# Kernel optimization log

Hardware: AMD Instinct MI355X
Metric: run time of the kernel (lower is better)

Reference implementation:

```python
import jax, jax.numpy as jnp
import numpy as np

D_MODEL = 1024
NUM_HEADS = 16
HDIM = D_MODEL // NUM_HEADS
THETA = 10000.0


def setup_inputs() -> dict:
    key = jax.random.key(0)
    ks = jax.random.split(key, 5)
    bs, seq = 4, 2048
    std = np.sqrt(2.0 / (D_MODEL + D_MODEL))
    def w(k):
        # trunc_normal approximated by clipped normal (same distribution family)
        return jnp.clip(std * jax.random.normal(k, (D_MODEL, D_MODEL), jnp.float32), -3 * std, 3 * std)
    return {
        "x": jax.random.normal(ks[0], (bs, seq, D_MODEL), jnp.float32),
        "Wq": w(ks[1]), "Wk": w(ks[2]), "Wv": w(ks[3]), "Wo": w(ks[4]),
        "token_positions": jnp.arange(seq, dtype=jnp.int64),
    }


def _rope(x, token_positions):
    # x: (bs, H, S, hdim); rotate even/odd interleaved pairs
    inv_freq = THETA ** (-2.0 * jnp.arange(HDIM // 2, dtype=jnp.float32) / HDIM)
    freqs = token_positions.astype(jnp.float32)[:, None] * inv_freq[None, :]  # (S, hdim/2)
    cos, sin = jnp.cos(freqs), jnp.sin(freqs)
    x_even, x_odd = x[..., 0::2], x[..., 1::2]
    out_even = x_even * cos - x_odd * sin
    out_odd = x_odd * cos + x_even * sin
    # interleave back: stack on new last axis then reshape
    return jnp.stack([out_even, out_odd], axis=-1).reshape(x.shape)


def reference(x, Wq, Wk, Wv, Wo, token_positions):
    bs, seq, _ = x.shape
    q = (x @ Wq.T).reshape(bs, seq, NUM_HEADS, HDIM).transpose(0, 2, 1, 3)
    k = (x @ Wk.T).reshape(bs, seq, NUM_HEADS, HDIM).transpose(0, 2, 1, 3)
    v = (x @ Wv.T).reshape(bs, seq, NUM_HEADS, HDIM).transpose(0, 2, 1, 3)
    q = _rope(q, token_positions)
    k = _rope(k, token_positions)
    scores = jnp.einsum("bhsd,bhtd->bhst", q, k) / jnp.sqrt(jnp.float32(HDIM))
    mask = jnp.tril(jnp.ones((seq, seq), dtype=bool))
    scores = jnp.where(mask, scores, -jnp.inf)
    attn = jax.nn.softmax(scores, axis=-1)
    out = jnp.einsum("bhst,bhtd->bhsd", attn, v)
    out = out.transpose(0, 2, 1, 3).reshape(bs, seq, D_MODEL)
    return out @ Wo.T
```

## Files before the change

### kernel.cpp

```cpp
#include <hip/hip_runtime.h>
#include <hip/hip_fp16.h>

typedef _Float16 half8 __attribute__((ext_vector_type(8)));
typedef _Float16 half4 __attribute__((ext_vector_type(4)));
typedef _Float16 half2v __attribute__((ext_vector_type(2)));
typedef float f32x4 __attribute__((ext_vector_type(4)));

#define SEQ   2048
#define DM    1024
#define NH    16
#define HD    64
#define BSZ   4

__device__ __forceinline__ void gload16(const void* g, void* l) {
  __builtin_amdgcn_global_load_lds((const __attribute__((address_space(1))) void*)g,
                                   (__attribute__((address_space(3))) void*)l,
                                   16, 0, 0);
}

__global__ void cvt4(const float* __restrict__ src, _Float16* __restrict__ dst, int n4) {
  int i = blockIdx.x * blockDim.x + threadIdx.x;
  if (i < n4) {
    float4 v = ((const float4*)src)[i];
    half4 o = { (_Float16)v.x, (_Float16)v.y, (_Float16)v.z, (_Float16)v.w };
    ((half4*)dst)[i] = o;
  }
}

template<int MODE>
__global__ __launch_bounds__(256)
void gemm_hk(const _Float16* __restrict__ A, const _Float16* __restrict__ B,
             _Float16* __restrict__ oQ, _Float16* __restrict__ oK,
             _Float16* __restrict__ oVt, float* __restrict__ oF) {
  __shared__ _Float16 As[128*32];
  __shared__ _Float16 Bs[128*32];
  const int tid  = threadIdx.x;
  const int wid  = tid >> 6, lane = tid & 63;
  const int wm   = wid >> 1, wn = wid & 1;
  const int fr   = lane & 15, fg = lane >> 4;
  const long m0  = (long)blockIdx.x * 128;
  const long n0  = (long)blockIdx.y * 128;
  const int lrow = lane >> 2;
  const int lcol = (lane & 3) * 8;
  const _Float16* ga0 = A + (m0 + wid*32 + lrow) * 1024 + lcol;
  const _Float16* gb0 = B + (n0 + wid*32 + lrow) * 1024 + lcol;
  _Float16* lA = &As[wid*32*32];
  _Float16* lB = &Bs[wid*32*32];

  f32x4 acc[4][4] = {};

  for (int k0 = 0; k0 < 1024; k0 += 32) {
    gload16(ga0 + k0,             lA);
    gload16(ga0 + k0 + 16*1024,   lA + 16*32);
    gload16(gb0 + k0,             lB);
    gload16(gb0 + k0 + 16*1024,   lB + 16*32);
    __syncthreads();
    half8 af[4], bf[4];
#pragma unroll
    for (int i = 0; i < 4; ++i) {
      af[i] = *(const half8*)&As[(wm*64 + i*16 + fr)*32 + fg*8];
      bf[i] = *(const half8*)&Bs[(wn*64 + i*16 + fr)*32 + fg*8];
    }
#pragma unroll
    for (int i = 0; i < 4; ++i)
#pragma unroll
      for (int j = 0; j < 4; ++j)
        acc[i][j] = __builtin_amdgcn_mfma_f32_16x16x32_f16(af[i], bf[j], acc[i][j], 0, 0, 0);
    __syncthreads();
  }

  if (MODE == 0) {
    const int which = (int)(n0 >> 10);
    const int nloc0 = ((int)n0 & 1023) + wn*64;
#pragma unroll
    for (int i = 0; i < 4; ++i) {
      const long r0 = m0 + wm*64 + i*16 + fg*4;
      const int  bb = (int)(r0 >> 11);
      const int  s  = (int)(r0 & 2047);
#pragma unroll
      for (int j = 0; j < 4; ++j) {
        const int nl = nloc0 + j*16 + fr;
        const int h  = nl >> 6, d = nl & 63;
        const long bh = (long)(bb*NH + h);
        if (which == 0) {
#pragma unroll
          for (int r = 0; r < 4; ++r)
            oQ[(bh*SEQ + s + r)*HD + d] = (_Float16)(acc[i][j][r] * 0.125f);
        } else if (which == 1) {
#pragma unroll
          for (int r = 0; r < 4; ++r)
            oK[(bh*SEQ + s + r)*HD + d] = (_Float16)acc[i][j][r];
        } else {
          half4 pk = { (_Float16)acc[i][j][0], (_Float16)acc[i][j][1],
                       (_Float16)acc[i][j][2], (_Float16)acc[i][j][3] };
          *(half4*)&oVt[(bh*HD + d)*SEQ + s] = pk;
        }
      }
    }
  } else {
#pragma unroll
    for (int i = 0; i < 4; ++i) {
      const long r0 = m0 + wm*64 + i*16 + fg*4;
#pragma unroll
      for (int j = 0; j < 4; ++j) {
        const long col = n0 + wn*64 + j*16 + fr;
#pragma unroll
        for (int r = 0; r < 4; ++r)
          oF[(r0 + r)*DM + col] = acc[i][j][r];
      }
    }
  }
}

__global__ void rope_k(_Float16* __restrict__ Q, _Float16* __restrict__ K,
                       const int* __restrict__ tp) {
  const int t = blockIdx.x * blockDim.x + threadIdx.x;
  const int s = t >> 5, p = t & 31;
  _Float16* base = blockIdx.z ? K : Q;
  half2v* ptr = (half2v*)(base + ((long)blockIdx.y * SEQ + s) * HD) + p;
  half2v v = *ptr;
  const float pos = (float)tp[s];
  const float inv = exp2f(-0.41524101186f * (float)p);
  const float f = pos * inv;
  float sn, cs;
  __sincosf(f, &sn, &cs);
  const float xe = (float)v[0], xo = (float)v[1];
  half2v o = { (_Float16)(xe*cs - xo*sn), (_Float16)(xo*cs + xe*sn) };
  *ptr = o;
}

__global__ __launch_bounds__(256, 4)
void fattn(const _Float16* __restrict__ Q, const _Float16* __restrict__ K,
           const _Float16* __restrict__ Vt, _Float16* __restrict__ O) {
  __shared__ _Float16 Ks[2][64*64];
  __shared__ _Float16 Vs[2][64*64];
  __shared__ _Float16 Ps[4][16*64];
  const int tid = threadIdx.x, wid = tid >> 6, lane = tid & 63;
  const int fr = lane & 15, fg = lane >> 4;
  const int bh = blockIdx.x;
  const int b = bh >> 4, h = bh & 15;
  const int y = blockIdx.y;
  const int perm = (y < 4) ? (15 - y) : (y < 8) ? (y + 4) : (y < 12) ? (y - 4) : (15 - y);
  const int q0 = perm * 128;
  const int qw = q0 + wid * 32;
  const _Float16* Qb = Q + (long)bh * SEQ * HD;
  const _Float16* Kb = K + (long)bh * SEQ * HD;
  const _Float16* Vb = Vt + (long)bh * HD * SEQ;

  half8 qf[2][2];
#pragma unroll
  for (int s = 0; s < 2; ++s) {
    qf[s][0] = *(const half8*)&Qb[(qw + s*16 + fr)*HD + fg*8];
    qf[s][1] = *(const half8*)&Qb[(qw + s*16 + fr)*HD + 32 + fg*8];
  }

  f32x4 oaccT[2][4] = {};
  float m_s[2] = { -1e30f, -1e30f }, l_s[2] = { 0.f, 0.f };

  const int srow = lane >> 3;
  const int sc16 = (lane & 7) ^ srow;
  const int r1 = wid*16 + srow, r2 = r1 + 8;

  char* Pb = (char*)&Ps[wid][0];
  const int swp = (fr & 7) << 4;
  const int nt = q0/64 + 2;

  gload16(Kb + (long)r1*HD + sc16*8, &Ks[0][(wid*16)*64]);
  gload16(Kb + (long)r2*HD + sc16*8, &Ks[0][(wid*16 + 8)*64]);
  gload16(Vb + (long)r1*SEQ + sc16*8, &Vs[0][(wid*16)*64]);
  gload16(Vb + (long)r2*SEQ + sc16*8, &Vs[0][(wid*16 + 8)*64]);
  __syncthreads();

  int cur = 0;
  for (int t = 0; t < nt; ++t) {
    const int kv0 = t * 64;

    if (t + 1 < nt) {
      const int nkv = kv0 + 64;
      gload16(Kb + (long)(nkv + r1)*HD + sc16*8, &Ks[cur^1][(wid*16)*64]);
      gload16(Kb + (long)(nkv + r2)*HD + sc16*8, &Ks[cur^1][(wid*16 + 8)*64]);
      gload16(Vb + (long)r1*SEQ + nkv + sc16*8,  &Vs[cur^1][(wid*16)*64]);
      gload16(Vb + (long)r2*SEQ + nkv + sc16*8,  &Vs[cur^1][(wid*16 + 8)*64]);
    }

    const char* Kc = (const char*)&Ks[cur][0];
    const char* Vc = (const char*)&Vs[cur][0];

#pragma unroll
    for (int s = 0; s < 2; ++s) {
      const int qa = qw + s*16 + fr;

      f32x4 sa[4];
      __builtin_amdgcn_s_setprio(1);
#pragma unroll
      for (int n = 0; n < 4; ++n) {
        const int row = n*16 + fr;
        const int sw = (row & 7) << 4;
        const half8 k0v = *(const half8*)(Kc + row*128 + ((fg*16) ^ sw));
        const half8 k1v = *(const half8*)(Kc + row*128 + ((64 + fg*16) ^ sw));
        f32x4 z = {0.f, 0.f, 0.f, 0.f};
        z = __builtin_amdgcn_mfma_f32_16x16x32_f16(k0v, qf[s][0], z, 0, 0, 0);
        sa[n] = __builtin_amdgcn_mfma_f32_16x16x32_f16(k1v, qf[s][1], z, 0, 0, 0);
      }
      __builtin_amdgcn_s_setprio(0);

      if (kv0 + 63 > qw + s*16) {
#pragma unroll
        for (int n = 0; n < 4; ++n) {
          const int kvb = kv0 + n*16 + fg*4;
#pragma unroll
          for (int r = 0; r < 4; ++r)
            if (kvb + r > qa) sa[n][r] = -1e30f;
        }
      }

      float pm0 = fmaxf(fmaxf(sa[0][0], sa[0][1]), fmaxf(sa[0][2], sa[0][3]));
      float pm1 = fmaxf(fmaxf(sa[1][0], sa[1][1]), fmaxf(sa[1][2], sa[1][3]));
      float pm2 = fmaxf(fmaxf(sa[2][0], sa[2][1]), fmaxf(sa[2][2], sa[2][3]));
      float pm3 = fmaxf(fmaxf(sa[3][0], sa[3][1]), fmaxf(sa[3][2], sa[3][3]));
      float pm = fmaxf(fmaxf(pm0, pm1), fmaxf(pm2, pm3));
      pm = fmaxf(pm, __shfl_xor(pm, 16));
      pm = fmaxf(pm, __shfl_xor(pm, 32));

      const float mn = fmaxf(m_s[s], pm);
      const float fac = __expf(m_s[s] - mn);
      m_s[s] = mn;

      float ps = 0.f;
#pragma unroll
      for (int n = 0; n < 4; ++n)
#pragma unroll
        for (int r = 0; r < 4; ++r) {
          const float p = __expf(sa[n][r] - mn);
          sa[n][r] = p;
          ps += p;
        }
      ps += __shfl_xor(ps, 16);
      ps += __shfl_xor(ps, 32);
      l_s[s] = l_s[s]*fac + ps;

#pragma unroll
      for (int n = 0; n < 4; ++n) {
        oaccT[s][n][0] *= fac; oaccT[s][n][1] *= fac;
        oaccT[s][n][2] *= fac; oaccT[s][n][3] *= fac;
      }

#pragma unroll
      for (int n = 0; n < 4; ++n) {
        half4 p4 = { (_Float16)sa[n][0], (_Float16)sa[n][1],
                     (_Float16)sa[n][2], (_Float16)sa[n][3] };
        *(half4*)(Pb + ((fr*128 + n*32 + fg*8) ^ swp)) = p4;
      }

      __builtin_amdgcn_s_setprio(1);
#pragma unroll
      for (int ks = 0; ks < 2; ++ks) {
        const half8 pf = *(const half8*)(Pb + ((fr*128 + ks*64 + fg*16) ^ swp));
#pragma unroll
        for (int nd = 0; nd < 4; ++nd) {
          const int row = nd*16 + fr;
          const int sw = (row & 7) << 4;
          const half8 vf = *(const half8*)(Vc + row*128 + ((ks*64 + fg*16) ^ sw));
          oaccT[s][nd] = __builtin_amdgcn_mfma_f32_16x16x32_f16(vf, pf, oaccT[s][nd], 0, 0, 0);
        }
      }
      __builtin_amdgcn_s_setprio(0);
    }

    __syncthreads();
    cur ^= 1;
  }

#pragma unroll
  for (int s = 0; s < 2; ++s) {
    const float rl = __builtin_amdgcn_rcpf(l_s[s]);
    _Float16* orow = O + ((long)b*SEQ + (qw + s*16 + fr))*DM + h*64;
#pragma unroll
    for (int nd = 0; nd < 4; ++nd) {
      half4 o4 = { (_Float16)(oaccT[s][nd][0]*rl), (_Float16)(oaccT[s][nd][1]*rl),
                   (_Float16)(oaccT[s][nd][2]*rl), (_Float16)(oaccT[s][nd][3]*rl) };
      *(half4*)&orow[nd*16 + fg*4] = o4;
    }
  }
}

extern "C" void kernel_launch(void* const* d_in, const int* in_sizes, int n_in,
                              void* d_out, int out_size, void* d_ws, size_t ws_size,
                              hipStream_t stream) {
  const float* x  = (const float*)d_in[0];
  const float* Wq = (const float*)d_in[1];
  const float* Wk = (const float*)d_in[2];
  const float* Wv = (const float*)d_in[3];
  const float* Wo = (const float*)d_in[4];
  const int*   tp = (const int*)d_in[5];
  float* out = (float*)d_out;

  char* ws = (char*)d_ws;
  _Float16* xh   = (_Float16*)(ws);
  _Float16* Wqkv = (_Float16*)(ws + (16u << 20));
  _Float16* Woh  = (_Float16*)(ws + (22u << 20));
  _Float16* Qb   = (_Float16*)(ws + (24u << 20));
  _Float16* Kb   = (_Float16*)(ws + (40u << 20));
  _Float16* Vtb  = (_Float16*)(ws + (56u << 20));
  _Float16* attn = (_Float16*)(ws + (72u << 20));

  cvt4<<<8192, 256, 0, stream>>>(x,  xh, 2097152);
  cvt4<<<1024, 256, 0, stream>>>(Wq, Wqkv,               262144);
  cvt4<<<1024, 256, 0, stream>>>(Wk, Wqkv + (1u << 20),  262144);
  cvt4<<<1024, 256, 0, stream>>>(Wv, Wqkv + (2u << 20),  262144);
  cvt4<<<1024, 256, 0, stream>>>(Wo, Woh,                262144);

  gemm_hk<0><<<dim3(64, 24), 256, 0, stream>>>(xh, Wqkv, Qb, Kb, Vtb, nullptr);
  rope_k<<<dim3(256, 64, 2), 256, 0, stream>>>(Qb, Kb, tp);
  fattn<<<dim3(64, 16), 256, 0, stream>>>(Qb, Kb, Vtb, attn);
  gemm_hk<1><<<dim3(64, 8), 256, 0, stream>>>(attn, Woh, nullptr, nullptr, nullptr, out);
}
```

Measured before the change: 200.2 us.

## Use exp2 softmax with lazy rescaling, hoisted K fragments and causal skip

Folds log2(e) into the Q scale so the softmax can use the hardware exp2 instead of expf. Rescaling of the output accumulator is skipped when the running max has not grown by more than a threshold (lazy rescale). K fragments are loaded from LDS once per tile and shared across both query sub-blocks, and fully masked sub-blocks are skipped. Packed f16 conversion (cvt_pkrtz) is used for P and the output. This trades fewer transcendental ops, fewer LDS reads and less rescaling work for a small accuracy risk from round-toward-zero conversion and from the bounded stale max, and it raises register pressure from the hoisted K fragments.

```diff
diff --git a/kernel.cpp b/kernel.cpp
--- a/kernel.cpp
+++ b/kernel.cpp
@@ -12,10 +12,25 @@
 #define HD    64
 #define BSZ   4
 
+#if __has_builtin(__builtin_amdgcn_exp2f)
+#define EXP2(x) __builtin_amdgcn_exp2f(x)
+#else
+#define EXP2(x) exp2f(x)
+#endif
+
+#define QSCALE 0.1803368801f
+
 __device__ __forceinline__ void gload16(const void* g, void* l) {
   __builtin_amdgcn_global_load_lds((const __attribute__((address_space(1))) void*)g,
                                    (__attribute__((address_space(3))) void*)l,
                                    16, 0, 0);
+}
+
+__device__ __forceinline__ f32x4 vmax4(f32x4 a, f32x4 b) {
+  f32x4 r;
+  r[0] = fmaxf(a[0], b[0]); r[1] = fmaxf(a[1], b[1]);
+  r[2] = fmaxf(a[2], b[2]); r[3] = fmaxf(a[3], b[3]);
+  return r;
 }
 
 __global__ void cvt4(const float* __restrict__ src, _Float16* __restrict__ dst, int n4) {
@@ -85,7 +100,7 @@
         if (which == 0) {
 #pragma unroll
           for (int r = 0; r < 4; ++r)
-            oQ[(bh*SEQ + s + r)*HD + d] = (_Float16)(acc[i][j][r] * 0.125f);
+            oQ[(bh*SEQ + s + r)*HD + d] = (_Float16)(acc[i][j][r] * QSCALE);
         } else if (which == 1) {
 #pragma unroll
           for (int r = 0; r < 4; ++r)
@@ -186,25 +201,32 @@
     const char* Kc = (const char*)&Ks[cur][0];
     const char* Vc = (const char*)&Vs[cur][0];
 
+    half8 kf0[4], kf1[4];
+#pragma unroll
+    for (int n = 0; n < 4; ++n) {
+      const int row = n*16 + fr;
+      const int sw = (row & 7) << 4;
+      kf0[n] = *(const half8*)(Kc + row*128 + ((fg*16) ^ sw));
+      kf1[n] = *(const half8*)(Kc + row*128 + ((64 + fg*16) ^ sw));
+    }
+
 #pragma unroll
     for (int s = 0; s < 2; ++s) {
-      const int qa = qw + s*16 + fr;
+      const int qs0 = qw + s*16;
+      if (kv0 > qs0 + 15) continue;
+      const int qa = qs0 + fr;
 
       f32x4 sa[4];
       __builtin_amdgcn_s_setprio(1);
 #pragma unroll
       for (int n = 0; n < 4; ++n) {
-        const int row = n*16 + fr;
-        const int sw = (row & 7) << 4;
-        const half8 k0v = *(const half8*)(Kc + row*128 + ((fg*16) ^ sw));
-        const half8 k1v = *(const half8*)(Kc + row*128 + ((64 + fg*16) ^ sw));
         f32x4 z = {0.f, 0.f, 0.f, 0.f};
-        z = __builtin_amdgcn_mfma_f32_16x16x32_f16(k0v, qf[s][0], z, 0, 0, 0);
-        sa[n] = __builtin_amdgcn_mfma_f32_16x16x32_f16(k1v, qf[s][1], z, 0, 0, 0);
+        z = __builtin_amdgcn_mfma_f32_16x16x32_f16(kf0[n], qf[s][0], z, 0, 0, 0);
+        sa[n] = __builtin_amdgcn_mfma_f32_16x16x32_f16(kf1[n], qf[s][1], z, 0, 0, 0);
       }
       __builtin_amdgcn_s_setprio(0);
 
-      if (kv0 + 63 > qw + s*16) {
+      if (kv0 + 63 > qs0) {
 #pragma unroll
         for (int n = 0; n < 4; ++n) {
           const int kvb = kv0 + n*16 + fg*4;
@@ -214,41 +236,38 @@
         }
       }
 
-      float pm0 = fmaxf(fmaxf(sa[0][0], sa[0][1]), fmaxf(sa[0][2], sa[0][3]));
-      float pm1 = fmaxf(fmaxf(sa[1][0], sa[1][1]), fmaxf(sa[1][2], sa[1][3]));
-      float pm2 = fmaxf(fmaxf(sa[2][0], sa[2][1]), fmaxf(sa[2][2], sa[2][3]));
-      float pm3 = fmaxf(fmaxf(sa[3][0], sa[3][1]), fmaxf(sa[3][2], sa[3][3]));
-      float pm = fmaxf(fmaxf(pm0, pm1), fmaxf(pm2, pm3));
+      f32x4 mx = vmax4(vmax4(sa[0], sa[1]), vmax4(sa[2], sa[3]));
+      float pm = fmaxf(fmaxf(mx[0], mx[1]), fmaxf(mx[2], mx[3]));
       pm = fmaxf(pm, __shfl_xor(pm, 16));
       pm = fmaxf(pm, __shfl_xor(pm, 32));
 
-      const float mn = fmaxf(m_s[s], pm);
-      const float fac = __expf(m_s[s] - mn);
-      m_s[s] = mn;
-
-      float ps = 0.f;
+      if (!__all(pm <= m_s[s] + 8.0f)) {
+        const float mn = fmaxf(m_s[s], pm);
+        const float fac = EXP2(m_s[s] - mn);
+        m_s[s] = mn;
+        l_s[s] *= fac;
+#pragma unroll
+        for (int n = 0; n < 4; ++n) oaccT[s][n] *= fac;
+      }
+      const float mrow = m_s[s];
+
 #pragma unroll
       for (int n = 0; n < 4; ++n)
 #pragma unroll
-        for (int r = 0; r < 4; ++r) {
-          const float p = __expf(sa[n][r] - mn);
-          sa[n][r] = p;
-          ps += p;
-        }
+        for (int r = 0; r < 4; ++r)
+          sa[n][r] = EXP2(sa[n][r] - mrow);
+
+      f32x4 s4 = (sa[0] + sa[1]) + (sa[2] + sa[3]);
+      float ps = (s4[0] + s4[1]) + (s4[2] + s4[3]);
       ps += __shfl_xor(ps, 16);
       ps += __shfl_xor(ps, 32);
-      l_s[s] = l_s[s]*fac + ps;
+      l_s[s] += ps;
 
 #pragma unroll
       for (int n = 0; n < 4; ++n) {
-        oaccT[s][n][0] *= fac; oaccT[s][n][1] *= fac;
-        oaccT[s][n][2] *= fac; oaccT[s][n][3] *= fac;
-      }
-
-#pragma unroll
-      for (int n = 0; n < 4; ++n) {
-        half4 p4 = { (_Float16)sa[n][0], (_Float16)sa[n][1],
-                     (_Float16)sa[n][2], (_Float16)sa[n][3] };
+        half2v lo = (half2v)__builtin_amdgcn_cvt_pkrtz(sa[n][0], sa[n][1]);
+        half2v hi = (half2v)__builtin_amdgcn_cvt_pkrtz(sa[n][2], sa[n][3]);
+        half4 p4 = __builtin_shufflevector(lo, hi, 0, 1, 2, 3);
         *(half4*)(Pb + ((fr*128 + n*32 + fg*8) ^ swp)) = p4;
       }
 
@@ -277,8 +296,9 @@
     _Float16* orow = O + ((long)b*SEQ + (qw + s*16 + fr))*DM + h*64;
 #pragma unroll
     for (int nd = 0; nd < 4; ++nd) {
-      half4 o4 = { (_Float16)(oaccT[s][nd][0]*rl), (_Float16)(oaccT[s][nd][1]*rl),
-                   (_Float16)(oaccT[s][nd][2]*rl), (_Float16)(oaccT[s][nd][3]*rl) };
+      half2v lo = (half2v)__builtin_amdgcn_cvt_pkrtz(oaccT[s][nd][0]*rl, oaccT[s][nd][1]*rl);
+      half2v hi = (half2v)__builtin_amdgcn_cvt_pkrtz(oaccT[s][nd][2]*rl, oaccT[s][nd][3]*rl);
+      half4 o4 = __builtin_shufflevector(lo, hi, 0, 1, 2, 3);
       *(half4*)&orow[nd*16 + fg*4] = o4;
     }
   }
```

Result: slower. 219.2 us (+9.5%).
